# Kernel optimization log

Measured on AMD Instinct MI355X. Metric: run time of the kernel, lower is better.

The kernel has to match this reference:

```python
import jax, jax.numpy as jnp
import numpy as np

DIN = 2048
DOUT = 2048
NUM_HEADS = 16
HEAD_DIM = DIN // NUM_HEADS  # 128
BLOCK_SIZE = 2048
ROPE_THETA = 10000.0


def precompute_freqs(block_size, head_dim):
    inv_freq = 1.0 / (ROPE_THETA ** (jnp.arange(0, head_dim, 2, dtype=jnp.float32) / head_dim))
    t = jnp.arange(block_size, dtype=jnp.float32)
    freqs = jnp.outer(t, inv_freq)  # [S, head_dim//2]
    return jnp.cos(freqs), jnp.sin(freqs)


def apply_rotary_emb(x, cos, sin):
    # x: [B, S, H, D]; cos/sin: [S, D//2]
    xr = x.reshape(*x.shape[:-1], -1, 2)  # pairs of consecutive dims (complex view)
    x1, x2 = xr[..., 0], xr[..., 1]
    c = cos[None, :, None, :]
    s = sin[None, :, None, :]
    o1 = x1 * c - x2 * s
    o2 = x1 * s + x2 * c
    return jnp.stack([o1, o2], axis=-1).reshape(x.shape)


def setup_inputs() -> dict:
    key = jax.random.key(0)
    k1, k2, k3 = jax.random.split(key, 3)
    x = jax.random.normal(k1, (2, 2048, DIN), dtype=jnp.float32)
    Wqkv = jax.random.normal(k2, (DIN, 3 * DOUT), dtype=jnp.float32) * (DIN ** -0.5)
    Wproj = jax.random.normal(k3, (DIN, DOUT), dtype=jnp.float32) * (DIN ** -0.5)
    return {"x": x, "Wqkv": Wqkv, "Wproj": Wproj}


def reference(x, Wqkv, Wproj):
    B, S, _ = x.shape
    cos, sin = precompute_freqs(BLOCK_SIZE, HEAD_DIM)
    cos, sin = cos[:S], sin[:S]
    qkv = x @ Wqkv  # [B, S, 3*DOUT]
    q, k, v = jnp.split(qkv, 3, axis=-1)
    q = q.reshape(B, S, NUM_HEADS, HEAD_DIM)
    k = k.reshape(B, S, NUM_HEADS, HEAD_DIM)
    v = v.reshape(B, S, NUM_HEADS, HEAD_DIM)
    q = apply_rotary_emb(q, cos, sin)
    k = apply_rotary_emb(k, cos, sin)
    # causal SDPA with scale 1/sqrt(head_dim)
    scale = HEAD_DIM ** -0.5
    scores = jnp.einsum('bqhd,bkhd->bhqk', q, k) * scale
    causal = jnp.tril(jnp.ones((S, S), dtype=bool))
    scores = jnp.where(causal[None, None], scores, jnp.finfo(scores.dtype).min)
    attn = jax.nn.softmax(scores, axis=-1)
    y = jnp.einsum('bhqk,bkhd->bqhd', attn, v).reshape(B, S, DOUT)
    return y @ Wproj
```

## Files before the change

### kernel.cpp

```cpp
#include <hip/hip_runtime.h>

#define DIN 2048
#define NH 16
#define DH 128
#define SEQ 2048
#define BB 2
#define N3 6144
#define MM 4096

typedef __bf16 bf16;
typedef __attribute__((ext_vector_type(8))) __bf16 bf16x8;
typedef __attribute__((ext_vector_type(4))) __bf16 bf16x4;
typedef __attribute__((ext_vector_type(2))) __bf16 bf16x2;
typedef __attribute__((ext_vector_type(4))) float f32x4;

__device__ __forceinline__ f32x4 mfma16(bf16x8 a, bf16x8 b, f32x4 c) {
  return __builtin_amdgcn_mfma_f32_16x16x32_bf16(a, b, c, 0, 0, 0);
}

__device__ __forceinline__ void async16(const void* g, void* l) {
  __builtin_amdgcn_global_load_lds((const __attribute__((address_space(1))) void*)g,
                                   (__attribute__((address_space(3))) void*)l, 16, 0, 0);
}

__global__ void sniff_k(const unsigned short* __restrict__ x, int* __restrict__ flag) {
  __shared__ int cnt;
  if (threadIdx.x == 0) cnt = 0;
  __syncthreads();
  unsigned short u = x[threadIdx.x * 2];
  int e = (u >> 7) & 0xff;
  if (e >= 108 && e <= 140) atomicAdd(&cnt, 1);
  __syncthreads();
  if (threadIdx.x == 0) *flag = (cnt >= 128) ? 1 : 0;
}

__global__ __launch_bounds__(256) void trig_k(float2* __restrict__ trig) {
  int i = blockIdx.x * 256 + threadIdx.x;
  int d2 = i & 63, s = i >> 6;
  float invf = expf(-9.210340371976184f * (float)(2 * d2) * (1.0f / 128.0f));
  float sn, cs;
  sincosf((float)s * invf, &sn, &cs);
  trig[i] = make_float2(cs, sn);
}

__global__ __launch_bounds__(256) void cast_x_k(const void* __restrict__ in, bf16* __restrict__ out,
                                                const int* __restrict__ flag) {
  size_t i = ((size_t)blockIdx.x * 256 + threadIdx.x) * 8;
  if (*flag) {
    *(bf16x8*)(out + i) = *(const bf16x8*)((const bf16*)in + i);
  } else {
    const float* f = (const float*)in;
    bf16x8 v;
    for (int j = 0; j < 8; j++) v[j] = (bf16)f[i + j];
    *(bf16x8*)(out + i) = v;
  }
}

__global__ __launch_bounds__(256) void cast_wT_k(const void* __restrict__ in, bf16* __restrict__ out,
                                                 const int* __restrict__ flag, int R, int C) {
  __shared__ float t[32][33];
  int c0 = blockIdx.x * 32, r0 = blockIdx.y * 32;
  int tx = threadIdx.x & 31, ty = threadIdx.x >> 5;
  bool isb = *flag != 0;
  for (int j = 0; j < 4; j++) {
    int r = ty + j * 8;
    size_t idx = (size_t)(r0 + r) * C + c0 + tx;
    float v = isb ? (float)((const bf16*)in)[idx] : ((const float*)in)[idx];
    t[r][tx] = v;
  }
  __syncthreads();
  int tx8 = threadIdx.x & 15;
  int cy = threadIdx.x >> 4;
  for (int j = 0; j < 2; j++) {
    int c = cy + j * 16;
    bf16x2 v;
    v[0] = (bf16)t[2 * tx8][c];
    v[1] = (bf16)t[2 * tx8 + 1][c];
    *(bf16x2*)&out[(size_t)(c0 + c) * R + r0 + 2 * tx8] = v;
  }
}

__global__ __launch_bounds__(256) void gemm_qkv_k(const bf16* __restrict__ A, const bf16* __restrict__ BT,
                                                  bf16* __restrict__ Qb, bf16* __restrict__ Kb,
                                                  bf16* __restrict__ Vt,
                                                  const float2* __restrict__ trig, int m0base) {
  __shared__ __align__(16) bf16 As[128 * 64];
  __shared__ __align__(16) bf16 Bs[128 * 64];
  const int K = DIN;
  int m0 = m0base + blockIdx.y * 128, n0 = blockIdx.x * 128;
  int tid = threadIdx.x, w = tid >> 6, l = tid & 63;
  int l15 = l & 15, quad = l >> 4;
  int wm = (w & 1) * 64, wn = (w >> 1) * 64;
  f32x4 zero = {0.f, 0.f, 0.f, 0.f};
  f32x4 acc[4][4];
  for (int i = 0; i < 4; i++)
    for (int j = 0; j < 4; j++) acc[i][j] = zero;
  int gch = (l & 7) ^ (l >> 3);
  const bf16* Ag = A + (size_t)(m0 + w * 32 + (l >> 3)) * K + gch * 8;
  const bf16* Bg = BT + (size_t)(n0 + w * 32 + (l >> 3)) * K + gch * 8;
  bf16* AsW = As + w * 2048;
  bf16* BsW = Bs + w * 2048;
  for (int k0 = 0; k0 < K; k0 += 64) {
    __syncthreads();
    for (int j = 0; j < 4; j++) async16(Ag + k0 + (size_t)j * 8 * K, AsW + j * 512);
    for (int j = 0; j < 4; j++) async16(Bg + k0 + (size_t)j * 8 * K, BsW + j * 512);
    __syncthreads();
    for (int kk = 0; kk < 2; kk++) {
      bf16x8 af[4], bfv[4];
      for (int i = 0; i < 4; i++)
        af[i] = *(const bf16x8*)&As[(wm + i * 16 + l15) * 64 + (((kk * 4 + quad) ^ (l15 & 7)) << 3)];
      for (int j = 0; j < 4; j++)
        bfv[j] = *(const bf16x8*)&Bs[(wn + j * 16 + l15) * 64 + (((kk * 4 + quad) ^ (l15 & 7)) << 3)];
      for (int i = 0; i < 4; i++)
        for (int j = 0; j < 4; j++) acc[i][j] = mfma16(af[i], bfv[j], acc[i][j]);
    }
  }
  for (int j = 0; j < 4; j++) {
    int col = n0 + wn + j * 16 + l15;
    int part = col >> 11, cw = col & 2047;
    int h = cw >> 7, d = cw & 127;
    if (part < 2) {
      bf16* dst = (part == 0) ? Qb : Kb;
      int d2 = d >> 1;
      bool isodd = (d & 1) != 0;
      const float qscale = 0.08838834764831845f * 1.4426950408889634f;
      float sc = (part == 0) ? qscale : 1.0f;
      for (int i = 0; i < 4; i++) {
        int mrow = m0 + wm + i * 16 + quad * 4;
        for (int r = 0; r < 4; r++) {
          int m = mrow + r;
          int b = m >> 11, s = m & 2047;
          float v = acc[i][j][r];
          float p = __shfl_xor(v, 1, 64);
          float2 t = trig[(s << 6) + d2];
          float o = isodd ? (p * t.y + v * t.x) : (v * t.x - p * t.y);
          int dd = (part == 1) ? ((((d >> 3) ^ (s & 7)) << 3) | (d & 7)) : d;
          dst[(((size_t)(b * NH + h)) * SEQ + s) * DH + dd] = (bf16)(o * sc);
        }
      }
    } else {
      for (int i = 0; i < 4; i++) {
        int mrow = m0 + wm + i * 16 + quad * 4;
        int b = mrow >> 11, s = mrow & 2047;
        int scol = (s & ~63) | (((((s >> 3) & 7) ^ (d & 7)) << 3) | (s & 7));
        bf16x4 pk;
        for (int r = 0; r < 4; r++) pk[r] = (bf16)acc[i][j][r];
        *(bf16x4*)&Vt[((size_t)(b * NH + h) * DH + d) * SEQ + scol] = pk;
      }
    }
  }
}

__global__ __launch_bounds__(256, 2) void attn_k(const bf16* __restrict__ Qb, const bf16* __restrict__ Kb,
                                                 const bf16* __restrict__ Vt, bf16* __restrict__ Yb) {
  __shared__ __align__(16) bf16 Ks[2][64 * 128];
  __shared__ __align__(16) bf16 Vs[2][128 * 64];
  __shared__ __align__(16) bf16 Pl[4][16 * 76];
  int bh = blockIdx.x;
  int slot = blockIdx.y;
  int w = threadIdx.x >> 6, l = threadIdx.x & 63;
  int l15 = l & 15, quad = l >> 4;
  const bf16* Qp = Qb + (size_t)bh * SEQ * DH;
  const bf16* Kp = Kb + (size_t)bh * SEQ * DH;
  const bf16* Vp = Vt + (size_t)bh * DH * SEQ;
  int b = bh >> 4, h = bh & 15;
  f32x4 zero = {0.f, 0.f, 0.f, 0.f};
  bf16* P = &Pl[w][0];

  auto stage = [&](int it, int buf) {
    const char* gk = (const char*)Kp + (size_t)it * 16384 + w * 4096 + l * 16;
    char* lk = (char*)&Ks[buf][0] + w * 4096;
    for (int i = 0; i < 4; i++) async16(gk + i * 1024, lk + i * 1024);
    const char* gv = (const char*)Vp + (size_t)it * 128 + (size_t)(w * 32 + (l >> 3)) * (SEQ * 2) + (l & 7) * 16;
    char* lv = (char*)&Vs[buf][0] + w * 32 * 128;
    for (int i = 0; i < 4; i++) async16(gv + (size_t)i * 8 * (SEQ * 2), lv + i * 1024);
  };

  int tiles[2] = {31 - slot, slot};
  for (int half = 0; half < 2; half++) {
    int tile = tiles[half];
    int qw = tile * 64 + w * 16;
    bf16x8 qf[4];
    for (int kc = 0; kc < 4; kc++)
      qf[kc] = *(const bf16x8*)&Qp[(size_t)(qw + l15) * DH + kc * 32 + quad * 8];
    f32x4 o[8];
    for (int ns = 0; ns < 8; ns++) o[ns] = zero;
    float mprev = -1e30f, lsum = 0.f;
    int nkt = tile + 1;

    stage(0, 0);
    __syncthreads();
    for (int it = 0; it < nkt; it++) {
      int buf = it & 1;
      bool more = (it + 1 < nkt);
      asm volatile("s_waitcnt vmcnt(4)" ::: "memory");
      __builtin_amdgcn_s_barrier();
      __builtin_amdgcn_sched_barrier(0);
      if (more) stage(it + 1, buf ^ 1);
      int k0 = it * 64;
      f32x4 st[4];
      for (int ns = 0; ns < 4; ns++) st[ns] = zero;
      __builtin_amdgcn_s_setprio(1);
      for (int kc = 0; kc < 4; kc++)
        for (int ns = 0; ns < 4; ns++) {
          bf16x8 kf = *(const bf16x8*)&Ks[buf][(ns * 16 + l15) * 128 + (((kc * 4 + quad) ^ (l15 & 7)) << 3)];
          st[ns] = mfma16(kf, qf[kc], st[ns]);
        }
      __builtin_amdgcn_s_setprio(0);
      int qq = qw + l15;
      if (k0 + 63 > qw) {
        for (int ns = 0; ns < 4; ns++) {
          int kk = k0 + ns * 16 + quad * 4;
          for (int r = 0; r < 4; r++)
            if (kk + r > qq) st[ns][r] = -1e30f;
        }
      }
      float pm = -1e30f;
      for (int ns = 0; ns < 4; ns++)
        for (int r = 0; r < 4; r++) pm = fmaxf(pm, st[ns][r]);
      pm = fmaxf(pm, __shfl_xor(pm, 16, 64));
      pm = fmaxf(pm, __shfl_xor(pm, 32, 64));
      float mnew = fmaxf(mprev, pm);
      float al = exp2f(mprev - mnew);
      mprev = mnew;
      float ps = 0.f;
      for (int ns = 0; ns < 4; ns++)
        for (int r = 0; r < 4; r++) {
          float e = exp2f(st[ns][r] - mnew);
          st[ns][r] = e;
          ps += e;
        }
      ps += __shfl_xor(ps, 16, 64);
      ps += __shfl_xor(ps, 32, 64);
      lsum = lsum * al + ps;
      for (int ns = 0; ns < 8; ns++) o[ns] *= al;
      for (int ns = 0; ns < 4; ns++) {
        bf16x4 pk;
        for (int r = 0; r < 4; r++) pk[r] = (bf16)st[ns][r];
        *(bf16x4*)&P[l15 * 76 + ns * 16 + quad * 4] = pk;
      }
      asm volatile("s_waitcnt lgkmcnt(0)" ::: "memory");
      bf16x8 pa[2];
      for (int kc = 0; kc < 2; kc++)
        pa[kc] = *(const bf16x8*)&P[l15 * 76 + kc * 32 + quad * 8];
      if (more) {
        asm volatile("s_waitcnt vmcnt(8)" ::: "memory");
      } else {
        asm volatile("s_waitcnt vmcnt(0)" ::: "memory");
      }
      __builtin_amdgcn_s_barrier();
      __builtin_amdgcn_sched_barrier(0);
      __builtin_amdgcn_s_setprio(1);
      for (int ns = 0; ns < 8; ns++)
        for (int kc = 0; kc < 2; kc++) {
          bf16x8 vf = *(const bf16x8*)&Vs[buf][(ns * 16 + l15) * 64 + (((kc * 4 + quad) ^ (l15 & 7)) << 3)];
          o[ns] = mfma16(vf, pa[kc], o[ns]);
        }
      __builtin_amdgcn_s_setprio(0);
    }
    __syncthreads();
    float inv = 1.0f / lsum;
    int q = qw + l15;
    size_t base = ((size_t)(b * SEQ + q)) * DIN + h * DH + quad * 4;
    for (int ns = 0; ns < 8; ns++) {
      bf16x4 pk;
      for (int r = 0; r < 4; r++) pk[r] = (bf16)(o[ns][r] * inv);
      *(bf16x4*)&Yb[base + ns * 16] = pk;
    }
  }
}

__global__ __launch_bounds__(256) void gemm_proj_k(const bf16* __restrict__ A, const bf16* __restrict__ BT,
                                                   void* __restrict__ out, const int* __restrict__ flag) {
  __shared__ __align__(16) bf16 As[128 * 64];
  __shared__ __align__(16) bf16 Bs[128 * 64];
  const int K = DIN;
  int m0 = blockIdx.y * 128, n0 = blockIdx.x * 128;
  int tid = threadIdx.x, w = tid >> 6, l = tid & 63;
  int l15 = l & 15, quad = l >> 4;
  int wm = (w & 1) * 64, wn = (w >> 1) * 64;
  bool obf = *flag != 0;
  f32x4 zero = {0.f, 0.f, 0.f, 0.f};
  f32x4 acc[4][4];
  for (int i = 0; i < 4; i++)
    for (int j = 0; j < 4; j++) acc[i][j] = zero;
  int gch = (l & 7) ^ (l >> 3);
  const bf16* Ag = A + (size_t)(m0 + w * 32 + (l >> 3)) * K + gch * 8;
  const bf16* Bg = BT + (size_t)(n0 + w * 32 + (l >> 3)) * K + gch * 8;
  bf16* AsW = As + w * 2048;
  bf16* BsW = Bs + w * 2048;
  for (int k0 = 0; k0 < K; k0 += 64) {
    __syncthreads();
    for (int j = 0; j < 4; j++) async16(Ag + k0 + (size_t)j * 8 * K, AsW + j * 512);
    for (int j = 0; j < 4; j++) async16(Bg + k0 + (size_t)j * 8 * K, BsW + j * 512);
    __syncthreads();
    for (int kk = 0; kk < 2; kk++) {
      bf16x8 af[4], bfv[4];
      for (int i = 0; i < 4; i++)
        af[i] = *(const bf16x8*)&As[(wm + i * 16 + l15) * 64 + (((kk * 4 + quad) ^ (l15 & 7)) << 3)];
      for (int j = 0; j < 4; j++)
        bfv[j] = *(const bf16x8*)&Bs[(wn + j * 16 + l15) * 64 + (((kk * 4 + quad) ^ (l15 & 7)) << 3)];
      for (int i = 0; i < 4; i++)
        for (int j = 0; j < 4; j++) acc[i][j] = mfma16(af[i], bfv[j], acc[i][j]);
    }
  }
  for (int j = 0; j < 4; j++) {
    int col = n0 + wn + j * 16 + l15;
    for (int i = 0; i < 4; i++) {
      int mrow = m0 + wm + i * 16 + quad * 4;
      for (int r = 0; r < 4; r++) {
        size_t idx = (size_t)(mrow + r) * DIN + col;
        float v = acc[i][j][r];
        if (obf)
          ((bf16*)out)[idx] = (bf16)v;
        else
          ((float*)out)[idx] = v;
      }
    }
  }
}

extern "C" void kernel_launch(void* const* d_in, const int* in_sizes, int n_in,
                              void* d_out, int out_size, void* d_ws, size_t ws_size,
                              hipStream_t stream) {
  char* ws = (char*)d_ws;
  int* flag = (int*)ws;
  bf16* Xb = (bf16*)(ws + 256);
  bf16* WqkvT = (bf16*)(ws + 256 + 16777216);
  bf16* WprojT = (bf16*)(ws + 256 + 16777216 + 25165824);
  bf16* Qb = (bf16*)(ws + 256 + 16777216 + 25165824 + 8388608);
  bf16* Kb = Qb + (size_t)MM * DIN;
  bf16* Vb = Kb + (size_t)MM * DIN;
  bf16* Vt = Vb + (size_t)MM * DIN;
  bf16* Yb = Xb;
  float2* trig = (float2*)Vb;

  sniff_k<<<1, 256, 0, stream>>>((const unsigned short*)d_in[0], flag);
  trig_k<<<512, 256, 0, stream>>>(trig);
  cast_x_k<<<4096, 256, 0, stream>>>(d_in[0], Xb, flag);
  cast_wT_k<<<dim3(192, 64), 256, 0, stream>>>(d_in[1], WqkvT, flag, DIN, N3);
  cast_wT_k<<<dim3(64, 64), 256, 0, stream>>>(d_in[2], WprojT, flag, DIN, DIN);
  gemm_qkv_k<<<dim3(48, 16), 256, 0, stream>>>(Xb, WqkvT, Qb, Kb, Vt, trig, 0);
  gemm_qkv_k<<<dim3(48, 16), 256, 0, stream>>>(Xb, WqkvT, Qb, Kb, Vt, trig, 2048);
  attn_k<<<dim3(32, 16), 256, 0, stream>>>(Qb, Kb, Vt, Yb);
  gemm_proj_k<<<dim3(16, 32), 256, 0, stream>>>(Yb, WprojT, d_out, flag);
}
```

Measured before the change: 419.5 us.

## Split RoPE out of QKV GEMM epilogue into separate LUT kernel

Removes the rotary embedding and the Q scaling from the QKV GEMM epilogue, so the GEMM writes raw bf16 Q/K. A new elementwise kernel reads Q and K back, applies the rotation from the trig table plus the Q scale, and writes them in place, honouring the swizzled K layout. The two half-M GEMM launches are merged into one 48x32 grid. This trades a lighter GEMM epilogue (no shuffles or trig loads) for an extra pass over Q and K in memory, plus an added bf16 rounding before the rotation.

```diff
diff --git a/kernel.cpp b/kernel.cpp
--- a/kernel.cpp
+++ b/kernel.cpp
@@ -82,12 +82,11 @@
 
 __global__ __launch_bounds__(256) void gemm_qkv_k(const bf16* __restrict__ A, const bf16* __restrict__ BT,
                                                   bf16* __restrict__ Qb, bf16* __restrict__ Kb,
-                                                  bf16* __restrict__ Vt,
-                                                  const float2* __restrict__ trig, int m0base) {
+                                                  bf16* __restrict__ Vt) {
   __shared__ __align__(16) bf16 As[128 * 64];
   __shared__ __align__(16) bf16 Bs[128 * 64];
   const int K = DIN;
-  int m0 = m0base + blockIdx.y * 128, n0 = blockIdx.x * 128;
+  int m0 = blockIdx.y * 128, n0 = blockIdx.x * 128;
   int tid = threadIdx.x, w = tid >> 6, l = tid & 63;
   int l15 = l & 15, quad = l >> 4;
   int wm = (w & 1) * 64, wn = (w >> 1) * 64;
@@ -121,21 +120,13 @@
     int h = cw >> 7, d = cw & 127;
     if (part < 2) {
       bf16* dst = (part == 0) ? Qb : Kb;
-      int d2 = d >> 1;
-      bool isodd = (d & 1) != 0;
-      const float qscale = 0.08838834764831845f * 1.4426950408889634f;
-      float sc = (part == 0) ? qscale : 1.0f;
       for (int i = 0; i < 4; i++) {
         int mrow = m0 + wm + i * 16 + quad * 4;
         for (int r = 0; r < 4; r++) {
           int m = mrow + r;
           int b = m >> 11, s = m & 2047;
-          float v = acc[i][j][r];
-          float p = __shfl_xor(v, 1, 64);
-          float2 t = trig[(s << 6) + d2];
-          float o = isodd ? (p * t.y + v * t.x) : (v * t.x - p * t.y);
           int dd = (part == 1) ? ((((d >> 3) ^ (s & 7)) << 3) | (d & 7)) : d;
-          dst[(((size_t)(b * NH + h)) * SEQ + s) * DH + dd] = (bf16)(o * sc);
+          dst[(((size_t)(b * NH + h)) * SEQ + s) * DH + dd] = (bf16)acc[i][j][r];
         }
       }
     } else {
@@ -148,6 +139,42 @@
         *(bf16x4*)&Vt[((size_t)(b * NH + h) * DH + d) * SEQ + scol] = pk;
       }
     }
+  }
+}
+
+__global__ __launch_bounds__(256) void rope_lut_k(bf16* __restrict__ Qb, bf16* __restrict__ Kb,
+                                                  const float2* __restrict__ trig) {
+  int i = blockIdx.x * 256 + threadIdx.x;
+  int g = i & 15;
+  int s = (i >> 4) & 2047;
+  int bh = i >> 15;
+  size_t row = ((size_t)bh * SEQ + s) * DH;
+  float2 tt[4];
+  for (int p = 0; p < 4; p++) tt[p] = trig[(s << 6) + 4 * g + p];
+  const float qscale = 0.08838834764831845f * 1.4426950408889634f;
+  {
+    bf16* qp = Qb + row + 8 * g;
+    bf16x8 v = *(const bf16x8*)qp;
+    bf16x8 o;
+#pragma unroll
+    for (int p = 0; p < 4; p++) {
+      float e = (float)v[2 * p], od = (float)v[2 * p + 1];
+      o[2 * p] = (bf16)((e * tt[p].x - od * tt[p].y) * qscale);
+      o[2 * p + 1] = (bf16)((e * tt[p].y + od * tt[p].x) * qscale);
+    }
+    *(bf16x8*)qp = o;
+  }
+  {
+    bf16* kp = Kb + row + ((g ^ (s & 7)) << 3);
+    bf16x8 v = *(const bf16x8*)kp;
+    bf16x8 o;
+#pragma unroll
+    for (int p = 0; p < 4; p++) {
+      float e = (float)v[2 * p], od = (float)v[2 * p + 1];
+      o[2 * p] = (bf16)(e * tt[p].x - od * tt[p].y);
+      o[2 * p + 1] = (bf16)(e * tt[p].y + od * tt[p].x);
+    }
+    *(bf16x8*)kp = o;
   }
 }
 
@@ -340,8 +367,8 @@
   cast_x_k<<<4096, 256, 0, stream>>>(d_in[0], Xb, flag);
   cast_wT_k<<<dim3(192, 64), 256, 0, stream>>>(d_in[1], WqkvT, flag, DIN, N3);
   cast_wT_k<<<dim3(64, 64), 256, 0, stream>>>(d_in[2], WprojT, flag, DIN, DIN);
-  gemm_qkv_k<<<dim3(48, 16), 256, 0, stream>>>(Xb, WqkvT, Qb, Kb, Vt, trig, 0);
-  gemm_qkv_k<<<dim3(48, 16), 256, 0, stream>>>(Xb, WqkvT, Qb, Kb, Vt, trig, 2048);
+  gemm_qkv_k<<<dim3(48, 32), 256, 0, stream>>>(Xb, WqkvT, Qb, Kb, Vt);
+  rope_lut_k<<<4096, 256, 0, stream>>>(Qb, Kb, trig);
   attn_k<<<dim3(32, 16), 256, 0, stream>>>(Qb, Kb, Vt, Yb);
   gemm_proj_k<<<dim3(16, 32), 256, 0, stream>>>(Yb, WprojT, d_out, flag);
 }
```

After: 396.8 us. -5.4%, faster.
